# Kernel optimization log

Hardware: AMD Instinct MI355X
Metric: run time of the kernel (lower is better)

The kernel has to match this reference:

```python
import jax, jax.numpy as jnp
import numpy as np

WS = 7  # window_size

def idct_matrix(N, dtype=jnp.float32):
    # scipy.fftpack.idct type-2 (no norm): y[n] = x[0] + 2*sum_{k>=1} x[k] cos(pi*k*(2n+1)/(2N))
    n = jnp.arange(N, dtype=dtype)[:, None]
    k = jnp.arange(N, dtype=dtype)[None, :]
    M = 2.0 * jnp.cos(jnp.pi * (2.0 * n + 1.0) * k / (2.0 * N))
    return M.at[:, 0].set(1.0)

def setup_inputs() -> dict:
    key = jax.random.key(0)
    k1, k2 = jax.random.split(key)
    B, H, W = 8, 384, 384
    X = jax.random.normal(k1, (B, H, W, WS * WS - 1), dtype=jnp.float32)
    im_zero_freq = jax.random.normal(k2, (B, H, W, 1), dtype=jnp.float32)
    return {"X": X, "im_zero_freq": im_zero_freq}

def reference(X, im_zero_freq):
    B, H, W, _ = X.shape
    ws = WS
    P, Q = H - ws, W - ws  # loop ranges: range(H-ws), range(W-ws)
    # Patch coefficient vector at (i,j): [zero_freq, high_freq...] -> (ws, ws)
    coeff = jnp.concatenate([im_zero_freq[:, :P, :Q, :], X[:, :P, :Q, :]], axis=-1)
    coeff = coeff.reshape(B, P, Q, ws, ws)
    M = idct_matrix(ws).astype(X.dtype)
    # 2D IDCT (axis 1 then axis 2 of each patch) as two small matmuls
    patches = jnp.einsum('nu,mv,bpquv->bpqnm', M, M, coeff)  # [B,P,Q,ws,ws]
    # Overwrite semantics: pixel (y,x) keeps the value from the LAST patch that
    # covered it, i.e. patch (min(y,P-1), min(x,Q-1)). Rows/cols beyond H-2/W-2
    # are never written and stay zero.
    y = jnp.arange(H)
    x = jnp.arange(W)
    i_sel = jnp.minimum(y, P - 1)
    j_sel = jnp.minimum(x, Q - 1)
    dy = y - i_sel  # offset within the selected patch, in [0, ws-1]
    dx = x - j_sel
    out = patches[:, i_sel[:, None], j_sel[None, :], dy[:, None], dx[None, :]]  # [B,H,W]
    valid = (y[:, None] <= H - 2) & (x[None, :] <= W - 2)
    out = jnp.where(valid[None, :, :], out, jnp.zeros((), dtype=out.dtype))
    return out[..., None]  # [B,H,W,1]
```

## Files before the change

kernel.cpp:

```cpp
#include <hip/hip_runtime.h>

#define WS 7
#define BB 8
#define HH 384
#define WW 384
#define PP 377
#define NC 48
#define NTOT (BB*HH*WW)

__constant__ float d_M[7][7] = {
    { 1.0f,  1.9498558244f,  1.8019377358f,  1.5636629649f,  1.2469796037f,  0.8677674782f,  0.4450418679f },
    { 1.0f,  1.5636629649f,  0.4450418679f, -0.8677674782f, -1.8019377358f, -1.9498558244f, -1.2469796037f },
    { 1.0f,  0.8677674782f, -1.2469796037f, -1.9498558244f, -0.4450418679f,  1.5636629649f,  1.8019377358f },
    { 1.0f,  0.0f,          -2.0f,           0.0f,           2.0f,           0.0f,          -2.0f          },
    { 1.0f, -0.8677674782f, -1.2469796037f,  1.9498558244f, -0.4450418679f, -1.5636629649f,  1.8019377358f },
    { 1.0f, -1.5636629649f,  0.4450418679f,  0.8677674782f, -1.8019377358f,  1.9498558244f, -1.2469796037f },
    { 1.0f, -1.9498558244f,  1.8019377358f, -1.5636629649f,  1.2469796037f, -0.8677674782f,  0.4450418679f },
};

__global__ __launch_bounds__(256) void idct_conv_kernel(
    const float* __restrict__ X,
    const float* __restrict__ zf,
    float* __restrict__ out)
{
    int tid = blockIdx.x * 256 + threadIdx.x;
    if (tid >= NTOT) return;

    int x   = tid % WW;
    int rem = tid / WW;
    int y   = rem % HH;
    int b   = rem / HH;

    if (y == HH - 1 || x == WW - 1) { out[tid] = 0.0f; return; }

    int i  = min(y, PP - 1);
    int j  = min(x, PP - 1);
    int dy = y - i;
    int dx = x - j;

    size_t base = ((size_t)b * HH + i) * WW + j;

    float c[49];
    c[0] = zf[base];
    const float4* xp = (const float4*)(X + base * NC);
#pragma unroll
    for (int q = 0; q < 12; ++q) {
        float4 v = xp[q];
        c[1 + 4*q] = v.x;
        c[2 + 4*q] = v.y;
        c[3 + 4*q] = v.z;
        c[4 + 4*q] = v.w;
    }

    const float* wu = d_M[dy];
    const float* wv = d_M[dx];

    float acc = 0.0f;
#pragma unroll
    for (int u = 0; u < 7; ++u) {
        float s = 0.0f;
#pragma unroll
        for (int v = 0; v < 7; ++v)
            s = fmaf(wv[v], c[u * 7 + v], s);
        acc = fmaf(wu[u], s, acc);
    }

    out[tid] = acc;
}

extern "C" void kernel_launch(void* const* d_in, const int* in_sizes, int n_in,
                              void* d_out, int out_size, void* d_ws, size_t ws_size,
                              hipStream_t stream) {
    const float* X  = (const float*)d_in[0];
    const float* zf = (const float*)d_in[1];
    float* out = (float*)d_out;

    const int threads = 256;
    const int blocks  = (NTOT + threads - 1) / threads;
    idct_conv_kernel<<<blocks, threads, 0, stream>>>(X, zf, out);
}
```

Baseline: 305.1 us.

## Stage each output row's coefficients in LDS via coalesced row-wide loads

Launch one 384-thread block per output row. Cooperatively load the row's 48-channel coefficients plus the zero-frequency term into shared memory with a padded stride of 49, then have each thread compute its pixel from shared memory. This replaces per-thread strided float4 reads, which coalesce poorly, with contiguous block-wide loads. The trade-offs are large per-block shared memory use, which limits occupancy, and a barrier before compute.

```diff
diff --git a/kernel.cpp b/kernel.cpp
--- a/kernel.cpp
+++ b/kernel.cpp
@@ -6,54 +6,62 @@
 #define WW 384
 #define PP 377
 #define NC 48
-#define NTOT (BB*HH*WW)
+#define STRIDE 49
+#define NSITE PP
+#define NX4 (PP * 12)
 
-__constant__ float d_M[7][7] = {
-    { 1.0f,  1.9498558244f,  1.8019377358f,  1.5636629649f,  1.2469796037f,  0.8677674782f,  0.4450418679f },
-    { 1.0f,  1.5636629649f,  0.4450418679f, -0.8677674782f, -1.8019377358f, -1.9498558244f, -1.2469796037f },
-    { 1.0f,  0.8677674782f, -1.2469796037f, -1.9498558244f, -0.4450418679f,  1.5636629649f,  1.8019377358f },
-    { 1.0f,  0.0f,          -2.0f,           0.0f,           2.0f,           0.0f,          -2.0f          },
-    { 1.0f, -0.8677674782f, -1.2469796037f,  1.9498558244f, -0.4450418679f, -1.5636629649f,  1.8019377358f },
-    { 1.0f, -1.5636629649f,  0.4450418679f,  0.8677674782f, -1.8019377358f,  1.9498558244f, -1.2469796037f },
-    { 1.0f, -1.9498558244f,  1.8019377358f, -1.5636629649f,  1.2469796037f, -0.8677674782f,  0.4450418679f },
+__constant__ float d_M[49] = {
+    1.0f,  1.9498558244f,  1.8019377358f,  1.5636629649f,  1.2469796037f,  0.8677674782f,  0.4450418679f,
+    1.0f,  1.5636629649f,  0.4450418679f, -0.8677674782f, -1.8019377358f, -1.9498558244f, -1.2469796037f,
+    1.0f,  0.8677674782f, -1.2469796037f, -1.9498558244f, -0.4450418679f,  1.5636629649f,  1.8019377358f,
+    1.0f,  0.0f,          -2.0f,           0.0f,           2.0f,           0.0f,          -2.0f,
+    1.0f, -0.8677674782f, -1.2469796037f,  1.9498558244f, -0.4450418679f, -1.5636629649f,  1.8019377358f,
+    1.0f, -1.5636629649f,  0.4450418679f,  0.8677674782f, -1.8019377358f,  1.9498558244f, -1.2469796037f,
+    1.0f, -1.9498558244f,  1.8019377358f, -1.5636629649f,  1.2469796037f, -0.8677674782f,  0.4450418679f,
 };
 
-__global__ __launch_bounds__(256) void idct_conv_kernel(
+__global__ __launch_bounds__(384) void idct_row_kernel(
     const float* __restrict__ X,
     const float* __restrict__ zf,
     float* __restrict__ out)
 {
-    int tid = blockIdx.x * 256 + threadIdx.x;
-    if (tid >= NTOT) return;
+    __shared__ float lds[NSITE * STRIDE];
+    __shared__ float ldsM[49];
 
-    int x   = tid % WW;
-    int rem = tid / WW;
-    int y   = rem % HH;
-    int b   = rem / HH;
+    const int t   = threadIdx.x;
+    const int row = blockIdx.x;
+    const int y   = row % HH;
+    const int b   = row / HH;
 
-    if (y == HH - 1 || x == WW - 1) { out[tid] = 0.0f; return; }
+    const size_t obase = (size_t)row * WW;
 
-    int i  = min(y, PP - 1);
-    int j  = min(x, PP - 1);
-    int dy = y - i;
-    int dx = x - j;
+    if (y == HH - 1) { out[obase + t] = 0.0f; return; }
 
-    size_t base = ((size_t)b * HH + i) * WW + j;
+    const int i = min(y, PP - 1);
+    const size_t rbase = ((size_t)b * HH + i) * WW;
+    const float4* __restrict__ xrow = (const float4*)(X + rbase * NC);
 
-    float c[49];
-    c[0] = zf[base];
-    const float4* xp = (const float4*)(X + base * NC);
-#pragma unroll
-    for (int q = 0; q < 12; ++q) {
-        float4 v = xp[q];
-        c[1 + 4*q] = v.x;
-        c[2 + 4*q] = v.y;
-        c[3 + 4*q] = v.z;
-        c[4 + 4*q] = v.w;
+    if (t < 49) ldsM[t] = d_M[t];
+
+    for (int q = t; q < NX4; q += 384) {
+        float4 v = xrow[q];
+        int j = q / 12;
+        int m = q - j * 12;
+        float* dst = &lds[j * STRIDE + 1 + 4 * m];
+        dst[0] = v.x; dst[1] = v.y; dst[2] = v.z; dst[3] = v.w;
     }
+    if (t < NSITE) lds[t * STRIDE] = zf[rbase + t];
 
-    const float* wu = d_M[dy];
-    const float* wv = d_M[dx];
+    __syncthreads();
+
+    const int x  = t;
+    const int j  = min(x, PP - 1);
+    const int dx = x - j;
+    const int dy = y - i;
+
+    const float* c  = &lds[j * STRIDE];
+    const float* wu = &ldsM[dy * 7];
+    const float* wv = &ldsM[dx * 7];
 
     float acc = 0.0f;
 #pragma unroll
@@ -65,7 +73,8 @@
         acc = fmaf(wu[u], s, acc);
     }
 
-    out[tid] = acc;
+    if (x == WW - 1) acc = 0.0f;
+    out[obase + x] = acc;
 }
 
 extern "C" void kernel_launch(void* const* d_in, const int* in_sizes, int n_in,
@@ -75,7 +84,5 @@
     const float* zf = (const float*)d_in[1];
     float* out = (float*)d_out;
 
-    const int threads = 256;
-    const int blocks  = (NTOT + threads - 1) / threads;
-    idct_conv_kernel<<<blocks, threads, 0, stream>>>(X, zf, out);
+    idct_row_kernel<<<BB * HH, 384, 0, stream>>>(X, zf, out);
 }
```

Result: slower. 340.9 us (+11.7%).
